# Optimization experiments

Measured on AMD Instinct MI355X. Metric: run time of the kernel, lower is better.

The kernel has to match this reference:

```python
import jax, jax.numpy as jnp
import numpy as np

ALPHA = 0.025
BETA = 0.00025
V_TH = 1.0
EXP_TAU = 50.0          # tau_v / dt
T_NOW = 10.0            # current simulation step counter self.t
REFRAC_STEPS = 2        # refractory_period / dt
INV_TAU_V = float(np.exp(-1.0 / 50.0))   # exp(-dt/tau_v)
INV_TAU_I = float(np.exp(-1.0))          # exp(-dt/tau_i)
INV_TAU_V_PAIR = INV_TAU_V               # tau_v_pair defaults to tau_v
INV_TAU_I_PAIR = INV_TAU_I               # tau_i_pair defaults to tau_i

B, N = 32, 4096


def setup_inputs() -> dict:
    key = jax.random.key(0)
    ks = jax.random.split(key, 8)
    return {
        "inp": jax.random.normal(ks[0], (B, N), jnp.float32),
        "W_rec": jax.random.uniform(ks[1], (N, N), jnp.float32),  # nonneg dense adjacency weights
        "mem_pot": jax.random.normal(ks[2], (B, N), jnp.float32),
        "mem_cur": jax.random.normal(ks[3], (B, N), jnp.float32),
        "mem_pot_paired": jax.random.normal(ks[4], (B, N), jnp.float32),
        "mem_cur_paired": jax.random.normal(ks[5], (B, N), jnp.float32),
        "st": jnp.zeros((N,), jnp.float32),
        "refrac_neurons": jax.random.randint(ks[6], (B, N), 0, 3, jnp.int32),
    }


def reference(inp, W_rec, mem_pot, mem_cur, mem_pot_paired, mem_cur_paired, st, refrac_neurons):
    sign_mask = W_rec > 0  # torch: sign(W_rec) > 0 (weights are nonneg)

    # decrement refractory counters
    refrac = jnp.where(refrac_neurons > 0, refrac_neurons - 1, refrac_neurons)

    # threshold (ceil+clamp -> {0,1} spikes)
    S = jnp.clip(jnp.ceil(mem_pot - V_TH), 0.0, 1.0)                     # (B,N)
    S_paired = jnp.clip(jnp.ceil(mem_pot_paired - V_TH - ALPHA), 0.0, 1.0)

    # ---- plasticity weight update ----
    sp_max = S_paired.max(axis=0)            # (N,)
    st_new = jnp.where(S > 0, T_NOW, st)     # broadcasts (N,) -> (B,N), as in torch
    max_st = st_new.max(axis=0)              # (N,)
    # meshgrid(a,b) with ij indexing: |a-b|[i,j] = |max_st[i]-max_st[j]|
    diff = jnp.abs(max_st[:, None] - max_st[None, :])                    # (N,N)
    update_mask = (sp_max[:, None] > 0) & sign_mask                      # (N,N)
    updated = W_rec + BETA - jnp.where(update_mask,
                                       ALPHA * jnp.exp(diff / EXP_TAU),
                                       0.0)
    updated = jnp.clip(updated, 0.0, 1.0)
    W_new = jnp.where(sign_mask, updated, W_rec)

    # ---- integrate ----
    active = refrac == 0
    mem_cur_n = jnp.where(active, inp + S @ W_new + mem_cur, mem_cur)
    mem_cur_p_n = jnp.where(active, S @ W_new.T + mem_cur_paired, mem_cur_paired)
    mem_pot_n = jnp.where(active, mem_cur_n + mem_pot, mem_pot)
    mem_pot_p_n = jnp.where(active, mem_cur_p_n + mem_pot_paired, mem_pot_paired)

    # leak
    mem_pot_n = mem_pot_n * INV_TAU_V
    mem_cur_n = mem_cur_n * INV_TAU_I
    mem_pot_p_n = mem_pot_p_n * INV_TAU_V_PAIR
    mem_cur_p_n = mem_cur_p_n * INV_TAU_I_PAIR

    # reset spiked neurons
    mem_pot_n = jnp.where(S > 0, 0.0, mem_pot_n)
    mem_pot_p_n = jnp.where(S_paired > 0, 0.0, mem_pot_p_n)
    refrac_new = jnp.where(S > 0, REFRAC_STEPS, refrac)

    return S, mem_pot_n, W_new, mem_cur_n, mem_pot_p_n, mem_cur_p_n, refrac_new
```

## Files before the change

### kernel.cpp

```cpp
#include <hip/hip_runtime.h>
#include <cstdint>
#include <cstddef>

constexpr int N = 4096;
constexpr int B = 32;
constexpr int BN = B * N;
constexpr size_t NN = (size_t)N * N;

constexpr int JCH = 8;
constexpr int JC = N / JCH;
constexpr int KCH = 8;
constexpr int KC = N / KCH;

constexpr float ALPHA = 0.025f;
constexpr float BETA = 0.00025f;
constexpr float T_NOW = 10.0f;
constexpr float INV_EXP_TAU = 0.02f;
constexpr float INV_TAU_V = 0.98019867f;
constexpr float INV_TAU_I = 0.36787944f;

typedef __attribute__((ext_vector_type(8))) short short8;
typedef __attribute__((ext_vector_type(4))) float f32x4;

__device__ inline unsigned short f2bf(float f) {
  uint32_t u = __float_as_uint(f);
  u += 0x7FFFu + ((u >> 16) & 1u);
  return (unsigned short)(u >> 16);
}

__global__ __launch_bounds__(256) void pass_a(
    const float* __restrict__ mem_pot, const float* __restrict__ mem_pot_p,
    const float* __restrict__ st, float* __restrict__ S_out,
    unsigned short* __restrict__ S_bf,
    uint32_t* __restrict__ maskS, uint32_t* __restrict__ maskSP,
    float* __restrict__ max_st, float* __restrict__ rowfac) {
  int j = blockIdx.x * blockDim.x + threadIdx.x;
  if (j >= N) return;
  float stj = st[j];
  uint32_t ms = 0u, msp = 0u;
  float maxv = -3.0e38f;
  #pragma unroll
  for (int b = 0; b < B; ++b) {
    float p = mem_pot[b * N + j];
    float pp = mem_pot_p[b * N + j];
    bool s = (p - 1.0f) > 0.0f;
    bool sp = ((pp - 1.0f) - ALPHA) > 0.0f;
    S_out[b * N + j] = s ? 1.0f : 0.0f;
    S_bf[b * N + j] = s ? 0x3F80u : 0u;
    ms |= (uint32_t)s << b;
    msp |= (uint32_t)sp << b;
    maxv = fmaxf(maxv, s ? T_NOW : stj);
  }
  maskS[j] = ms;
  maskSP[j] = msp;
  max_st[j] = maxv;
  rowfac[j] = msp ? ALPHA : 0.0f;
}

__global__ __launch_bounds__(256) void pass_b(
    const float* __restrict__ W, const unsigned short* __restrict__ S_bf,
    const float* __restrict__ max_st, const float* __restrict__ rowfac,
    float* __restrict__ Wout, float* __restrict__ partSWT) {
  int wv = threadIdx.x >> 6;
  int lane = threadIdx.x & 63;
  int nl = lane & 15;
  int quad = lane >> 4;
  int i = blockIdx.x * 64 + wv * 16 + nl;
  int jc = blockIdx.y;

  float mst_i = max_st[i];
  float fac_i = rowfac[i];
  const float* __restrict__ Wrow = W + (size_t)i * N;
  float* __restrict__ WoRow = Wout + (size_t)i * N;
  const unsigned short* __restrict__ A0p = S_bf + (size_t)nl * N;
  const unsigned short* __restrict__ A1p = S_bf + (size_t)(nl + 16) * N;

  f32x4 acc0 = {0.f, 0.f, 0.f, 0.f};
  f32x4 acc1 = {0.f, 0.f, 0.f, 0.f};

  auto upd = [&](float ww, float mstj) -> float {
    float d = fabsf(mst_i - mstj);
    float ex = __expf(d * INV_EXP_TAU);
    float u = ww + BETA - fac_i * ex;
    u = fminf(fmaxf(u, 0.0f), 1.0f);
    return (ww > 0.0f) ? u : ww;
  };

  #pragma unroll 2
  for (int it = 0; it < JC / 32; ++it) {
    int j = jc * JC + it * 32 + quad * 8;
    float4 w0 = *(const float4*)(Wrow + j);
    float4 w1 = *(const float4*)(Wrow + j + 4);
    float4 m0 = *(const float4*)(max_st + j);
    float4 m1 = *(const float4*)(max_st + j + 4);
    short8 a0 = *(const short8*)(A0p + j);
    short8 a1 = *(const short8*)(A1p + j);

    float4 o0, o1;
    o0.x = upd(w0.x, m0.x); o0.y = upd(w0.y, m0.y);
    o0.z = upd(w0.z, m0.z); o0.w = upd(w0.w, m0.w);
    o1.x = upd(w1.x, m1.x); o1.y = upd(w1.y, m1.y);
    o1.z = upd(w1.z, m1.z); o1.w = upd(w1.w, m1.w);
    *(float4*)(WoRow + j) = o0;
    *(float4*)(WoRow + j + 4) = o1;

    short8 bf;
    bf[0] = (short)f2bf(o0.x); bf[1] = (short)f2bf(o0.y);
    bf[2] = (short)f2bf(o0.z); bf[3] = (short)f2bf(o0.w);
    bf[4] = (short)f2bf(o1.x); bf[5] = (short)f2bf(o1.y);
    bf[6] = (short)f2bf(o1.z); bf[7] = (short)f2bf(o1.w);

    acc0 = __builtin_amdgcn_mfma_f32_16x16x32_bf16(a0, bf, acc0, 0, 0, 0);
    acc1 = __builtin_amdgcn_mfma_f32_16x16x32_bf16(a1, bf, acc1, 0, 0, 0);
  }

  size_t base = (size_t)jc * BN + (size_t)(blockIdx.x * 64 + wv * 16 + nl);
  #pragma unroll
  for (int r = 0; r < 4; ++r) {
    partSWT[base + (size_t)(quad * 4 + r) * N] = acc0[r];
    partSWT[base + (size_t)(16 + quad * 4 + r) * N] = acc1[r];
  }
}

__global__ __launch_bounds__(256) void pass_sw(
    const float* __restrict__ Wn, const unsigned short* __restrict__ S_bf,
    float* __restrict__ partSW) {
  int wv = threadIdx.x >> 6;
  int lane = threadIdx.x & 63;
  int ntile = blockIdx.x * 4 + wv;
  int j0 = ntile * 16;
  int kchunk = blockIdx.y;
  int kbase = kchunk * KC;
  int quad = lane >> 4;
  int nl = lane & 15;

  f32x4 acc0 = {0.f, 0.f, 0.f, 0.f};
  f32x4 acc1 = {0.f, 0.f, 0.f, 0.f};
  const unsigned short* __restrict__ A0p = S_bf + (size_t)nl * N;
  const unsigned short* __restrict__ A1p = S_bf + (size_t)(nl + 16) * N;

  #pragma unroll 4
  for (int it = 0; it < KC / 32; ++it) {
    int k0 = kbase + it * 32;
    short8 a0 = *(const short8*)(A0p + k0 + quad * 8);
    short8 a1 = *(const short8*)(A1p + k0 + quad * 8);
    short8 bf;
    #pragma unroll
    for (int i = 0; i < 8; ++i) {
      float f = Wn[(size_t)(k0 + quad * 8 + i) * N + j0 + nl];
      bf[i] = (short)f2bf(f);
    }
    acc0 = __builtin_amdgcn_mfma_f32_16x16x32_bf16(a0, bf, acc0, 0, 0, 0);
    acc1 = __builtin_amdgcn_mfma_f32_16x16x32_bf16(a1, bf, acc1, 0, 0, 0);
  }

  size_t base = (size_t)kchunk * BN + j0 + nl;
  #pragma unroll
  for (int r = 0; r < 4; ++r) {
    partSW[base + (size_t)(quad * 4 + r) * N] = acc0[r];
    partSW[base + (size_t)(16 + quad * 4 + r) * N] = acc1[r];
  }
}

__global__ __launch_bounds__(256) void pass_d(
    const float* __restrict__ inp, const float* __restrict__ mem_pot,
    const float* __restrict__ mem_cur, const float* __restrict__ mem_pot_p,
    const float* __restrict__ mem_cur_p, const int* __restrict__ refrac_in,
    const uint32_t* __restrict__ maskS, const uint32_t* __restrict__ maskSP,
    const float* __restrict__ partSW, const float* __restrict__ partSWT,
    float* __restrict__ pot_out, float* __restrict__ cur_out,
    float* __restrict__ potp_out, float* __restrict__ curp_out,
    float* __restrict__ refrac_out) {
  int e = blockIdx.x * 256 + threadIdx.x;
  int b = e >> 12;
  int j = e & (N - 1);

  float SW = 0.0f, SWT = 0.0f;
  #pragma unroll
  for (int c = 0; c < KCH; ++c) SW += partSW[(size_t)c * BN + e];
  #pragma unroll
  for (int c = 0; c < JCH; ++c) SWT += partSWT[(size_t)c * BN + e];

  int r = refrac_in[e];
  int rd = (r > 0) ? (r - 1) : r;
  bool active = (rd == 0);
  bool s = (maskS[j] >> b) & 1u;
  bool sp = (maskSP[j] >> b) & 1u;
  float cur = mem_cur[e], pot = mem_pot[e];
  float curp = mem_cur_p[e], potp = mem_pot_p[e];

  float cur_n = active ? (inp[e] + SW + cur) : cur;
  float curp_n = active ? (SWT + curp) : curp;
  float pot_n = active ? (cur_n + pot) : pot;
  float potp_n = active ? (curp_n + potp) : potp;

  pot_n *= INV_TAU_V;
  cur_n *= INV_TAU_I;
  potp_n *= INV_TAU_V;
  curp_n *= INV_TAU_I;

  if (s) pot_n = 0.0f;
  if (sp) potp_n = 0.0f;
  int rn = s ? 2 : rd;

  pot_out[e] = pot_n;
  cur_out[e] = cur_n;
  potp_out[e] = potp_n;
  curp_out[e] = curp_n;
  refrac_out[e] = (float)rn;
}

extern "C" void kernel_launch(void* const* d_in, const int* in_sizes, int n_in,
                              void* d_out, int out_size, void* d_ws, size_t ws_size,
                              hipStream_t stream) {
  const float* inp = (const float*)d_in[0];
  const float* W = (const float*)d_in[1];
  const float* mem_pot = (const float*)d_in[2];
  const float* mem_cur = (const float*)d_in[3];
  const float* mem_pot_p = (const float*)d_in[4];
  const float* mem_cur_p = (const float*)d_in[5];
  const float* st = (const float*)d_in[6];
  const int* refrac = (const int*)d_in[7];

  float* out = (float*)d_out;
  float* S_out = out;
  float* pot_out = out + BN;
  float* W_out = out + 2 * (size_t)BN;
  float* cur_out = W_out + NN;
  float* potp_out = cur_out + BN;
  float* curp_out = potp_out + BN;
  float* refrac_out = curp_out + BN;

  uint32_t* maskS = (uint32_t*)d_ws;
  uint32_t* maskSP = maskS + N;
  float* max_st = (float*)(maskSP + N);
  float* rowfac = max_st + N;
  unsigned short* S_bf = (unsigned short*)(rowfac + N);
  float* partSW = (float*)(S_bf + BN);
  float* partSWT = partSW + (size_t)KCH * BN;

  pass_a<<<N / 256, 256, 0, stream>>>(mem_pot, mem_pot_p, st, S_out, S_bf,
                                      maskS, maskSP, max_st, rowfac);
  pass_b<<<dim3(N / 64, JCH), 256, 0, stream>>>(W, S_bf, max_st, rowfac,
                                                W_out, partSWT);
  pass_sw<<<dim3(64, KCH), 256, 0, stream>>>(W_out, S_bf, partSW);
  pass_d<<<BN / 256, 256, 0, stream>>>(inp, mem_pot, mem_cur, mem_pot_p,
                                       mem_cur_p, refrac, maskS, maskSP,
                                       partSW, partSWT, pot_out, cur_out,
                                       potp_out, curp_out, refrac_out);
}
```

Measured before the change: 171.1 us.

## Restructure W update pass for more parallelism and stage transposed W tiles in LDS

pass_b now gives each block 16 rows, with the four waves splitting the j-chunk. All loads are issued up front, and the per-wave MFMA partials are reduced through shared memory. This gives 4x more blocks and more loads in flight. pass_sw replaces its strided per-element column reads of W_new with coalesced float4 row loads, a register prefetch, and a bf16 transpose into an LDS tile feeding the MFMAs. The costs are extra LDS traffic, block barriers, and a single-wave reduction epilogue in pass_b.

Measured after the change: 178.0 us. 4.0% more time.

```diff
diff --git a/kernel.cpp b/kernel.cpp
--- a/kernel.cpp
+++ b/kernel.cpp
@@ -65,7 +65,8 @@
   int lane = threadIdx.x & 63;
   int nl = lane & 15;
   int quad = lane >> 4;
-  int i = blockIdx.x * 64 + wv * 16 + nl;
+  int i0 = blockIdx.x * 16;
+  int i = i0 + nl;
   int jc = blockIdx.y;
 
   float mst_i = max_st[i];
@@ -74,6 +75,21 @@
   float* __restrict__ WoRow = Wout + (size_t)i * N;
   const unsigned short* __restrict__ A0p = S_bf + (size_t)nl * N;
   const unsigned short* __restrict__ A1p = S_bf + (size_t)(nl + 16) * N;
+
+  int jbase = jc * JC + wv * 128;
+
+  float4 w0[4], w1[4], m0[4], m1[4];
+  short8 a0[4], a1[4];
+  #pragma unroll
+  for (int it = 0; it < 4; ++it) {
+    int j = jbase + it * 32 + quad * 8;
+    w0[it] = *(const float4*)(Wrow + j);
+    w1[it] = *(const float4*)(Wrow + j + 4);
+    m0[it] = *(const float4*)(max_st + j);
+    m1[it] = *(const float4*)(max_st + j + 4);
+    a0[it] = *(const short8*)(A0p + j);
+    a1[it] = *(const short8*)(A1p + j);
+  }
 
   f32x4 acc0 = {0.f, 0.f, 0.f, 0.f};
   f32x4 acc1 = {0.f, 0.f, 0.f, 0.f};
@@ -86,21 +102,14 @@
     return (ww > 0.0f) ? u : ww;
   };
 
-  #pragma unroll 2
-  for (int it = 0; it < JC / 32; ++it) {
-    int j = jc * JC + it * 32 + quad * 8;
-    float4 w0 = *(const float4*)(Wrow + j);
-    float4 w1 = *(const float4*)(Wrow + j + 4);
-    float4 m0 = *(const float4*)(max_st + j);
-    float4 m1 = *(const float4*)(max_st + j + 4);
-    short8 a0 = *(const short8*)(A0p + j);
-    short8 a1 = *(const short8*)(A1p + j);
-
+  #pragma unroll
+  for (int it = 0; it < 4; ++it) {
+    int j = jbase + it * 32 + quad * 8;
     float4 o0, o1;
-    o0.x = upd(w0.x, m0.x); o0.y = upd(w0.y, m0.y);
-    o0.z = upd(w0.z, m0.z); o0.w = upd(w0.w, m0.w);
-    o1.x = upd(w1.x, m1.x); o1.y = upd(w1.y, m1.y);
-    o1.z = upd(w1.z, m1.z); o1.w = upd(w1.w, m1.w);
+    o0.x = upd(w0[it].x, m0[it].x); o0.y = upd(w0[it].y, m0[it].y);
+    o0.z = upd(w0[it].z, m0[it].z); o0.w = upd(w0[it].w, m0[it].w);
+    o1.x = upd(w1[it].x, m1[it].x); o1.y = upd(w1[it].y, m1[it].y);
+    o1.z = upd(w1[it].z, m1[it].z); o1.w = upd(w1[it].w, m1[it].w);
     *(float4*)(WoRow + j) = o0;
     *(float4*)(WoRow + j + 4) = o1;
 
@@ -110,55 +119,88 @@
     bf[4] = (short)f2bf(o1.x); bf[5] = (short)f2bf(o1.y);
     bf[6] = (short)f2bf(o1.z); bf[7] = (short)f2bf(o1.w);
 
-    acc0 = __builtin_amdgcn_mfma_f32_16x16x32_bf16(a0, bf, acc0, 0, 0, 0);
-    acc1 = __builtin_amdgcn_mfma_f32_16x16x32_bf16(a1, bf, acc1, 0, 0, 0);
-  }
-
-  size_t base = (size_t)jc * BN + (size_t)(blockIdx.x * 64 + wv * 16 + nl);
+    acc0 = __builtin_amdgcn_mfma_f32_16x16x32_bf16(a0[it], bf, acc0, 0, 0, 0);
+    acc1 = __builtin_amdgcn_mfma_f32_16x16x32_bf16(a1[it], bf, acc1, 0, 0, 0);
+  }
+
+  __shared__ float red[4][64][9];
   #pragma unroll
   for (int r = 0; r < 4; ++r) {
-    partSWT[base + (size_t)(quad * 4 + r) * N] = acc0[r];
-    partSWT[base + (size_t)(16 + quad * 4 + r) * N] = acc1[r];
+    red[wv][lane][r] = acc0[r];
+    red[wv][lane][r + 4] = acc1[r];
+  }
+  __syncthreads();
+  if (threadIdx.x < 64) {
+    int l = threadIdx.x;
+    int q = l >> 4, n = l & 15;
+    #pragma unroll
+    for (int r = 0; r < 8; ++r) {
+      float s = red[0][l][r] + red[1][l][r] + red[2][l][r] + red[3][l][r];
+      int b = (r < 4) ? (q * 4 + r) : (16 + q * 4 + (r - 4));
+      partSWT[(size_t)jc * BN + (size_t)b * N + i0 + n] = s;
+    }
   }
 }
 
 __global__ __launch_bounds__(256) void pass_sw(
     const float* __restrict__ Wn, const unsigned short* __restrict__ S_bf,
     float* __restrict__ partSW) {
-  int wv = threadIdx.x >> 6;
-  int lane = threadIdx.x & 63;
-  int ntile = blockIdx.x * 4 + wv;
-  int j0 = ntile * 16;
-  int kchunk = blockIdx.y;
-  int kbase = kchunk * KC;
+  __shared__ unsigned short tileT[64][72];
+
+  int t = threadIdx.x;
+  int wv = t >> 6;
+  int lane = t & 63;
+  int nl = lane & 15;
   int quad = lane >> 4;
-  int nl = lane & 15;
+  int j0 = blockIdx.x * 64;
+  int kc = blockIdx.y;
+  int kbase = kc * KC;
+
+  int r = t >> 2, q = t & 3;
+
+  const unsigned short* __restrict__ A0p = S_bf + (size_t)nl * N;
+  const unsigned short* __restrict__ A1p = S_bf + (size_t)(nl + 16) * N;
 
   f32x4 acc0 = {0.f, 0.f, 0.f, 0.f};
   f32x4 acc1 = {0.f, 0.f, 0.f, 0.f};
-  const unsigned short* __restrict__ A0p = S_bf + (size_t)nl * N;
-  const unsigned short* __restrict__ A1p = S_bf + (size_t)(nl + 16) * N;
-
-  #pragma unroll 4
-  for (int it = 0; it < KC / 32; ++it) {
-    int k0 = kbase + it * 32;
-    short8 a0 = *(const short8*)(A0p + k0 + quad * 8);
-    short8 a1 = *(const short8*)(A1p + k0 + quad * 8);
-    short8 bf;
+
+  const float* src = Wn + (size_t)(kbase + r) * N + j0 + q * 4;
+  float4 pf[4];
+  #pragma unroll
+  for (int f = 0; f < 4; ++f) pf[f] = *(const float4*)(src + f * 16);
+
+  for (int s = 0; s < KC / 64; ++s) {
+    __syncthreads();
     #pragma unroll
-    for (int i = 0; i < 8; ++i) {
-      float f = Wn[(size_t)(k0 + quad * 8 + i) * N + j0 + nl];
-      bf[i] = (short)f2bf(f);
-    }
-    acc0 = __builtin_amdgcn_mfma_f32_16x16x32_bf16(a0, bf, acc0, 0, 0, 0);
-    acc1 = __builtin_amdgcn_mfma_f32_16x16x32_bf16(a1, bf, acc1, 0, 0, 0);
-  }
-
-  size_t base = (size_t)kchunk * BN + j0 + nl;
-  #pragma unroll
-  for (int r = 0; r < 4; ++r) {
-    partSW[base + (size_t)(quad * 4 + r) * N] = acc0[r];
-    partSW[base + (size_t)(16 + quad * 4 + r) * N] = acc1[r];
+    for (int f = 0; f < 4; ++f) {
+      int c = q * 4 + f * 16;
+      tileT[c + 0][r] = f2bf(pf[f].x);
+      tileT[c + 1][r] = f2bf(pf[f].y);
+      tileT[c + 2][r] = f2bf(pf[f].z);
+      tileT[c + 3][r] = f2bf(pf[f].w);
+    }
+    if (s + 1 < KC / 64) {
+      src += (size_t)64 * N;
+      #pragma unroll
+      for (int f = 0; f < 4; ++f) pf[f] = *(const float4*)(src + f * 16);
+    }
+    __syncthreads();
+    #pragma unroll
+    for (int h = 0; h < 2; ++h) {
+      int k0 = kbase + s * 64 + h * 32;
+      short8 afr0 = *(const short8*)(A0p + k0 + quad * 8);
+      short8 afr1 = *(const short8*)(A1p + k0 + quad * 8);
+      short8 bfr = *(const short8*)(&tileT[wv * 16 + nl][h * 32 + quad * 8]);
+      acc0 = __builtin_amdgcn_mfma_f32_16x16x32_bf16(afr0, bfr, acc0, 0, 0, 0);
+      acc1 = __builtin_amdgcn_mfma_f32_16x16x32_bf16(afr1, bfr, acc1, 0, 0, 0);
+    }
+  }
+
+  size_t base = (size_t)kc * BN + j0 + wv * 16 + nl;
+  #pragma unroll
+  for (int rr = 0; rr < 4; ++rr) {
+    partSW[base + (size_t)(quad * 4 + rr) * N] = acc0[rr];
+    partSW[base + (size_t)(16 + quad * 4 + rr) * N] = acc1[rr];
   }
 }
 
@@ -241,7 +283,7 @@
 
   pass_a<<<N / 256, 256, 0, stream>>>(mem_pot, mem_pot_p, st, S_out, S_bf,
                                       maskS, maskSP, max_st, rowfac);
-  pass_b<<<dim3(N / 64, JCH), 256, 0, stream>>>(W, S_bf, max_st, rowfac,
+  pass_b<<<dim3(N / 16, JCH), 256, 0, stream>>>(W, S_bf, max_st, rowfac,
                                                 W_out, partSWT);
   pass_sw<<<dim3(64, KCH), 256, 0, stream>>>(W_out, S_bf, partSW);
   pass_d<<<BN / 256, 256, 0, stream>>>(inp, mem_pot, mem_cur, mem_pot_p,
```
